# Performance work log

Measured on AMD Instinct MI355X. Metric: run time of the kernel, lower is better.

The kernel has to match this reference:

```python
import jax, jax.numpy as jnp
import numpy as np

N, E = 20000, 320000
IN_CH, HID, NPRED = 64, 512, 12
NUM_GCN = 3   # num_gcn_layers=4 -> 1 + (4-2) layers
NUM_RNN = 2
BN_EPS = 1e-5


def setup_inputs() -> dict:
    key = jax.random.key(0)
    ks = jax.random.split(key, 16)
    s = 0.05  # init scale to keep activations sane
    return {
        "x": jax.random.normal(ks[0], (N, IN_CH), jnp.float32),
        "edge_index": jax.random.randint(ks[1], (2, E), 0, N, jnp.int32),
        "edge_weight": jax.random.uniform(ks[2], (E,), jnp.float32),
        "gcn0_W": jax.random.normal(ks[3], (IN_CH, HID), jnp.float32) * s,
        "gcn0_b": jnp.zeros((HID,), jnp.float32),
        "gcn_W": jax.random.normal(ks[4], (NUM_GCN - 1, HID, HID), jnp.float32) * s,
        "gcn_b": jnp.zeros((NUM_GCN - 1, HID), jnp.float32),
        "bn_gamma": jnp.ones((NUM_GCN, HID), jnp.float32),
        "bn_beta": jnp.zeros((NUM_GCN, HID), jnp.float32),
        "w_ih": jax.random.normal(ks[5], (NUM_RNN, HID, 4 * HID), jnp.float32) * s,
        "w_hh": jax.random.normal(ks[6], (NUM_RNN, HID, 4 * HID), jnp.float32) * s,
        "w_ch": jax.random.normal(ks[7], (NUM_RNN, HID, 3 * HID), jnp.float32) * s,
        "lstm_b": jnp.zeros((NUM_RNN, 4 * HID), jnp.float32),
        "out_W": jax.random.normal(ks[8], (HID, NPRED), jnp.float32) * s,
        "out_b": jnp.zeros((NPRED,), jnp.float32),
    }


def _gcn(x, W, b, src, dst, ew, n):
    h = x @ W                                   # [N, out]
    msg = ew[:, None] * h[src]                  # [E, out]
    return jax.ops.segment_sum(msg, dst, num_segments=n) + b


def _bn_relu(x, gamma, beta):
    mu = jnp.mean(x, axis=0)
    var = jnp.var(x, axis=0)
    return jax.nn.relu((x - mu) * jax.lax.rsqrt(var + BN_EPS) * gamma + beta)


def _peephole_cell(inp, h, c, Wih, Whh, Wch, b):
    H = h.shape[1]
    gates = inp @ Wih + h @ Whh + b             # [N, 4H]
    i_g, f_g, g_g, o_g = jnp.split(gates, 4, axis=1)
    g_g = g_g + c @ Wch[:, :H]
    i_g = jax.nn.sigmoid(i_g)
    f_g = jax.nn.sigmoid(f_g + c @ Wch[:, H:2 * H])
    g_g = jnp.tanh(g_g)
    cy = f_g * c + i_g * g_g
    o_g = o_g + cy @ Wch[:, 2 * H:]
    hy = jax.nn.sigmoid(o_g) * jnp.tanh(cy)
    return hy, cy


def reference(x, edge_index, edge_weight, gcn0_W, gcn0_b, gcn_W, gcn_b,
              bn_gamma, bn_beta, w_ih, w_hh, w_ch, lstm_b, out_W, out_b):
    src, dst = edge_index[0], edge_index[1]
    n = x.shape[0]
    # GCN stack: conv -> batchnorm (train-mode stats) -> relu (dropout=0)
    h = _gcn(x, gcn0_W, gcn0_b, src, dst, edge_weight, n)
    h = _bn_relu(h, bn_gamma[0], bn_beta[0])
    for i in range(NUM_GCN - 1):
        h = _gcn(h, gcn_W[i], gcn_b[i], src, dst, edge_weight, n)
        h = _bn_relu(h, bn_gamma[i + 1], bn_beta[i + 1])
    # seq_len == 1 after unsqueeze; cells chained sharing (h_t, c_t)
    h_t = jnp.zeros((n, HID), h.dtype)
    c_t = jnp.zeros((n, HID), h.dtype)
    for l in range(NUM_RNN):
        h_t, c_t = _peephole_cell(h, h_t, c_t, w_ih[l], w_hh[l], w_ch[l], lstm_b[l])
    out = h_t @ out_W + out_b                   # [N, num_predictions]
    return jnp.squeeze(out)
```

## Files before the change

kernel.cpp:

```cpp
#include <hip/hip_runtime.h>
#include <cstddef>

#define N_NODES 20000
#define N_EDGES 320000
#define IN_CH   64
#define HID     512
#define G4      2048
#define BN_EPS  1e-5f
#define F_OFF   0
#define G_OFF   512
#define I_OFF   1024
#define O_OFF   1536

typedef __attribute__((ext_vector_type(8))) __bf16 bf16x8;
typedef __attribute__((ext_vector_type(4))) float f32x4;

__device__ __forceinline__ float sigmoidf_(float x) {
  return 1.0f / (1.0f + expf(-x));
}

__device__ __forceinline__ unsigned short f2b(float f) {
  unsigned int u = __float_as_uint(f);
  u += 0x7FFFu + ((u >> 16) & 1u);
  return (unsigned short)(u >> 16);
}
__device__ __forceinline__ float b2f(unsigned short u) {
  return __uint_as_float(((unsigned int)u) << 16);
}

__device__ __forceinline__ void gld_lds16(const unsigned short* g, unsigned short* l) {
  __builtin_amdgcn_global_load_lds(
      (const __attribute__((address_space(1))) unsigned int*)(const void*)g,
      (__attribute__((address_space(3))) unsigned int*)(void*)l, 16, 0, 0);
}

__global__ __launch_bounds__(256) void zero_k(float* __restrict__ p, size_t n) {
  size_t i = ((size_t)blockIdx.x * 256 + threadIdx.x) * 4;
  if (i + 3 < n) {
    *(float4*)&p[i] = make_float4(0.f, 0.f, 0.f, 0.f);
  } else {
    for (; i < n; i++) p[i] = 0.f;
  }
}

struct TcvtDesc { const float* W; unsigned short* Wt; int K, NC, ldw, ldo; };
struct TcvtBatch { TcvtDesc d[18]; };

__global__ void tcvtb_k(TcvtBatch batch) {
  const TcvtDesc dd = batch.d[blockIdx.z];
  __shared__ float tile[32][33];
  const int n0 = blockIdx.x * 32, k0 = blockIdx.y * 32;
  if (n0 >= dd.NC || k0 >= dd.K) return;
  const int tx = threadIdx.x, ty = threadIdx.y;
  #pragma unroll
  for (int i = 0; i < 32; i += 8) {
    int k = k0 + ty + i, n = n0 + tx;
    tile[ty + i][tx] = (k < dd.K && n < dd.NC) ? dd.W[(size_t)k * dd.ldw + n] : 0.f;
  }
  __syncthreads();
  #pragma unroll
  for (int i = 0; i < 32; i += 8) {
    int n = n0 + ty + i, k = k0 + tx;
    if (n < dd.NC && k < dd.K) dd.Wt[(size_t)n * dd.ldo + k] = f2b(tile[tx][ty + i]);
  }
}

__global__ __launch_bounds__(256) void hist_k(const int* __restrict__ dst,
                                              int* __restrict__ counts) {
  int e = blockIdx.x * 256 + threadIdx.x;
  if (e < N_EDGES) atomicAdd(&counts[dst[e]], 1);
}

__global__ __launch_bounds__(128) void scan1_k(const int* __restrict__ counts,
                                               int* __restrict__ offsets,
                                               int* __restrict__ bsum, int n) {
  __shared__ int sh[128];
  const int b = blockIdx.x, t = threadIdx.x;
  const int i = b * 128 + t;
  const int v = (i < n) ? counts[i] : 0;
  sh[t] = v;
  __syncthreads();
  #pragma unroll
  for (int off = 1; off < 128; off <<= 1) {
    int u = (t >= off) ? sh[t - off] : 0;
    __syncthreads();
    sh[t] += u;
    __syncthreads();
  }
  if (i < n) offsets[i] = sh[t] - v;
  if (t == 127) bsum[b] = sh[127];
}

__global__ __launch_bounds__(128) void scan2_k(const int* __restrict__ bsum,
                                               int* __restrict__ offsets,
                                               int* __restrict__ pos,
                                               int n, int nb) {
  __shared__ int red[128];
  __shared__ int base_s;
  const int b = blockIdx.x, t = threadIdx.x;
  int part = 0;
  if (t < b) part += bsum[t];
  if (t + 128 < b) part += bsum[t + 128];
  red[t] = part;
  __syncthreads();
  if (t < 64) {
    int v = red[t] + red[t + 64];
    #pragma unroll
    for (int off = 32; off > 0; off >>= 1) v += __shfl_down(v, off);
    if (t == 0) base_s = v;
  }
  __syncthreads();
  const int i = b * 128 + t;
  if (i < n) {
    int off = base_s + offsets[i];
    offsets[i] = off;
    pos[i] = off;
  }
  if (b == nb - 1 && t == 0) offsets[n] = base_s + bsum[b];
}

__global__ __launch_bounds__(256) void fill_k(
    const int* __restrict__ src, const int* __restrict__ dst,
    const float* __restrict__ ew, int* __restrict__ pos,
    int* __restrict__ s_s, float* __restrict__ w_s) {
  int e = blockIdx.x * 256 + threadIdx.x;
  if (e >= N_EDGES) return;
  int p = atomicAdd(&pos[dst[e]], 1);
  s_s[p] = src[e];
  w_s[p] = ew[e];
}

__global__ __launch_bounds__(64) void gather64_k(
    const float* __restrict__ x, const int* __restrict__ offsets,
    const int* __restrict__ s_s, const float* __restrict__ w_s,
    unsigned short* __restrict__ xg) {
  const int sub = threadIdx.x >> 4;
  const int cg  = threadIdx.x & 15;
  const int n   = blockIdx.x * 4 + sub;
  const int beg = offsets[n], end = offsets[n + 1];
  float4 acc = make_float4(0.f, 0.f, 0.f, 0.f);
  int i = beg;
  for (; i + 3 < end; i += 4) {
    const int   s0 = s_s[i],     s1 = s_s[i + 1];
    const int   s2 = s_s[i + 2], s3 = s_s[i + 3];
    const float w0 = w_s[i],     w1 = w_s[i + 1];
    const float w2 = w_s[i + 2], w3 = w_s[i + 3];
    const float4 v0 = *(const float4*)&x[(size_t)s0 * IN_CH + cg * 4];
    const float4 v1 = *(const float4*)&x[(size_t)s1 * IN_CH + cg * 4];
    const float4 v2 = *(const float4*)&x[(size_t)s2 * IN_CH + cg * 4];
    const float4 v3 = *(const float4*)&x[(size_t)s3 * IN_CH + cg * 4];
    acc.x = fmaf(w0, v0.x, acc.x); acc.y = fmaf(w0, v0.y, acc.y);
    acc.z = fmaf(w0, v0.z, acc.z); acc.w = fmaf(w0, v0.w, acc.w);
    acc.x = fmaf(w1, v1.x, acc.x); acc.y = fmaf(w1, v1.y, acc.y);
    acc.z = fmaf(w1, v1.z, acc.z); acc.w = fmaf(w1, v1.w, acc.w);
    acc.x = fmaf(w2, v2.x, acc.x); acc.y = fmaf(w2, v2.y, acc.y);
    acc.z = fmaf(w2, v2.z, acc.z); acc.w = fmaf(w2, v2.w, acc.w);
    acc.x = fmaf(w3, v3.x, acc.x); acc.y = fmaf(w3, v3.y, acc.y);
    acc.z = fmaf(w3, v3.z, acc.z); acc.w = fmaf(w3, v3.w, acc.w);
  }
  for (; i < end; i++) {
    const int   s = s_s[i];
    const float w = w_s[i];
    const float4 v = *(const float4*)&x[(size_t)s * IN_CH + cg * 4];
    acc.x = fmaf(w, v.x, acc.x);
    acc.y = fmaf(w, v.y, acc.y);
    acc.z = fmaf(w, v.z, acc.z);
    acc.w = fmaf(w, v.w, acc.w);
  }
  ushort4 o; o.x = f2b(acc.x); o.y = f2b(acc.y); o.z = f2b(acc.z); o.w = f2b(acc.w);
  *(ushort4*)&xg[(size_t)n * IN_CH + cg * 4] = o;
}

__global__ __launch_bounds__(128) void gather_k(
    const unsigned short* __restrict__ XW, const int* __restrict__ offsets,
    const int* __restrict__ s_s, const float* __restrict__ w_s,
    unsigned short* __restrict__ H) {
  const int n = blockIdx.x;
  const int t = threadIdx.x;
  const int beg = offsets[n], end = offsets[n + 1];
  float4 acc = make_float4(0.f, 0.f, 0.f, 0.f);
  int i = beg;
  for (; i + 3 < end; i += 4) {
    const int   s0 = s_s[i],     s1 = s_s[i + 1];
    const int   s2 = s_s[i + 2], s3 = s_s[i + 3];
    const float w0 = w_s[i],     w1 = w_s[i + 1];
    const float w2 = w_s[i + 2], w3 = w_s[i + 3];
    const ushort4 v0 = *(const ushort4*)&XW[(size_t)s0 * HID + t * 4];
    const ushort4 v1 = *(const ushort4*)&XW[(size_t)s1 * HID + t * 4];
    const ushort4 v2 = *(const ushort4*)&XW[(size_t)s2 * HID + t * 4];
    const ushort4 v3 = *(const ushort4*)&XW[(size_t)s3 * HID + t * 4];
    acc.x = fmaf(w0, b2f(v0.x), acc.x); acc.y = fmaf(w0, b2f(v0.y), acc.y);
    acc.z = fmaf(w0, b2f(v0.z), acc.z); acc.w = fmaf(w0, b2f(v0.w), acc.w);
    acc.x = fmaf(w1, b2f(v1.x), acc.x); acc.y = fmaf(w1, b2f(v1.y), acc.y);
    acc.z = fmaf(w1, b2f(v1.z), acc.z); acc.w = fmaf(w1, b2f(v1.w), acc.w);
    acc.x = fmaf(w2, b2f(v2.x), acc.x); acc.y = fmaf(w2, b2f(v2.y), acc.y);
    acc.z = fmaf(w2, b2f(v2.z), acc.z); acc.w = fmaf(w2, b2f(v2.w), acc.w);
    acc.x = fmaf(w3, b2f(v3.x), acc.x); acc.y = fmaf(w3, b2f(v3.y), acc.y);
    acc.z = fmaf(w3, b2f(v3.z), acc.z); acc.w = fmaf(w3, b2f(v3.w), acc.w);
  }
  for (; i < end; i++) {
    const int   s = s_s[i];
    const float w = w_s[i];
    const ushort4 v = *(const ushort4*)&XW[(size_t)s * HID + t * 4];
    acc.x = fmaf(w, b2f(v.x), acc.x);
    acc.y = fmaf(w, b2f(v.y), acc.y);
    acc.z = fmaf(w, b2f(v.z), acc.z);
    acc.w = fmaf(w, b2f(v.w), acc.w);
  }
  ushort4 o; o.x = f2b(acc.x); o.y = f2b(acc.y); o.z = f2b(acc.z); o.w = f2b(acc.w);
  *(ushort4*)&H[(size_t)n * HID + t * 4] = o;
}

__global__ __launch_bounds__(256) void bn_stats_k(
    const unsigned short* __restrict__ H, float* __restrict__ stats, int N)
{
  const int tx = threadIdx.x & 63;
  const int ty = threadIdx.x >> 6;
  const int col = blockIdx.x * 64 + tx;
  float s1 = 0.f, s2 = 0.f;
  for (int r = blockIdx.y * 4 + ty; r < N; r += gridDim.y * 4) {
    float v = b2f(H[(size_t)r * HID + col]);
    s1 += v; s2 += v * v;
  }
  __shared__ float red[2][4][64];
  red[0][ty][tx] = s1;
  red[1][ty][tx] = s2;
  __syncthreads();
  if (ty == 0) {
    s1 = red[0][0][tx] + red[0][1][tx] + red[0][2][tx] + red[0][3][tx];
    s2 = red[1][0][tx] + red[1][1][tx] + red[1][2][tx] + red[1][3][tx];
    atomicAdd(&stats[col], s1);
    atomicAdd(&stats[HID + col], s2);
  }
}

__global__ __launch_bounds__(256) void bn_apply_k(
    const unsigned short* __restrict__ H, const float* __restrict__ stats,
    const float* __restrict__ gamma, const float* __restrict__ beta,
    unsigned short* __restrict__ out, int N)
{
  size_t gid = (size_t)blockIdx.x * 256 + threadIdx.x;
  size_t idx = gid * 4;
  if (idx >= (size_t)N * HID) return;
  int col = (int)(idx & (HID - 1));
  const ushort4 v = *(const ushort4*)&H[idx];
  float r[4] = {b2f(v.x), b2f(v.y), b2f(v.z), b2f(v.w)};
  ushort4 o;
  unsigned short* op = &o.x;
  #pragma unroll
  for (int i = 0; i < 4; i++) {
    int c = col + i;
    float mean = stats[c] * (1.0f / N);
    float var  = stats[HID + c] * (1.0f / N) - mean * mean;
    float scale = gamma[c] / sqrtf(var + BN_EPS);
    float shift = beta[c] - mean * scale;
    op[i] = f2b(fmaxf(fmaf(r[i], scale, shift), 0.0f));
  }
  *(ushort4*)&out[idx] = o;
}

template<int BM, int BN>
__global__ __launch_bounds__(256) void gemm_bf16_k(
    const unsigned short* __restrict__ A, int lda,
    const unsigned short* __restrict__ A2, int lda2, int ksplit,
    const unsigned short* __restrict__ Bt,
    float* __restrict__ C, unsigned short* __restrict__ C16,
    const float* __restrict__ bias,
    int M, int K, int Ksmall, int NC, int ldc, int acc, int ntc,
    int nrowb, int ncolb)
{
  const int b   = blockIdx.x;
  const int xcd = b & 7;
  const int j   = b >> 3;
  const int col_b = j % ncolb;
  const int row_b = (j / ncolb) * 8 + xcd;
  if (row_b >= nrowb) return;

  constexpr int MI  = 2;
  constexpr int ASZ = BM * 64;
  constexpr int BSZ = BN * 64;
  __shared__ unsigned short As[2 * ASZ];
  __shared__ unsigned short Bs[2 * BSZ];
  const int row0 = row_b * BM;
  const int col0 = col_b * BN;
  const int Kthis = (col0 < 1024) ? K : Ksmall;
  const int t    = threadIdx.x;
  const int lane = t & 63;
  const int w    = t >> 6;
  const int wro  = (BN == 128) ? (w >> 1) * 32 : w * 32;
  const int wco  = (BN == 128) ? (w & 1) * 64 : 0;
  const int q    = lane >> 4;
  const int l16  = lane & 15;

  f32x4 accr[MI][4] = {};

  auto stage = [&](int buf, int k0) {
    unsigned short* Ad = As + buf * ASZ;
    unsigned short* Bd = Bs + buf * BSZ;
    #pragma unroll
    for (int i = 0; i < BM / 32; i++) {
      int s  = t + i * 256;
      int r  = s >> 3, cq = s & 7;
      int kq = (cq - r) & 7;
      int gr = row0 + r; if (gr > M - 1) gr = M - 1;
      int kk = k0 + kq * 8;
      const unsigned short* bp = (kk < ksplit) ? A : A2;
      size_t off = (kk < ksplit) ? ((size_t)gr * lda + kk)
                                 : ((size_t)gr * lda2 + (kk - ksplit));
      gld_lds16(bp + off, Ad + (size_t)s * 8);
    }
    #pragma unroll
    for (int i = 0; i < BN / 32; i++) {
      int s  = t + i * 256;
      int r  = s >> 3, cq = s & 7;
      int kq = (cq - r) & 7;
      gld_lds16(Bt + (size_t)(col0 + r) * K + k0 + kq * 8, Bd + (size_t)s * 8);
    }
  };

  stage(0, 0);
  int cur = 0;
  for (int k0 = 0; k0 < Kthis; k0 += 64) {
    __syncthreads();
    if (k0 + 64 < Kthis) stage(cur ^ 1, k0 + 64);

    const unsigned short* Ac = As + cur * ASZ;
    const unsigned short* Bc = Bs + cur * BSZ;
    #pragma unroll
    for (int ks = 0; ks < 2; ks++) {
      bf16x8 af[MI], bfr[4];
      #pragma unroll
      for (int mi = 0; mi < MI; mi++) {
        int r = wro + mi * 16 + l16;
        int slot = (ks * 4 + q + r) & 7;
        af[mi] = *(const bf16x8*)&Ac[r * 64 + slot * 8];
      }
      #pragma unroll
      for (int ni = 0; ni < 4; ni++) {
        int r = wco + ni * 16 + l16;
        int slot = (ks * 4 + q + r) & 7;
        bfr[ni] = *(const bf16x8*)&Bc[r * 64 + slot * 8];
      }
      #pragma unroll
      for (int mi = 0; mi < MI; mi++)
        #pragma unroll
        for (int ni = 0; ni < 4; ni++)
          accr[mi][ni] = __builtin_amdgcn_mfma_f32_16x16x32_bf16(
              af[mi], bfr[ni], accr[mi][ni], 0, 0, 0);
    }
    cur ^= 1;
  }

  #pragma unroll
  for (int mi = 0; mi < MI; mi++) {
    #pragma unroll
    for (int ni = 0; ni < 4; ni++) {
      int col = col0 + wco + ni * 16 + l16;
      #pragma unroll
      for (int r = 0; r < 4; r++) {
        int row = row0 + wro + mi * 16 + q * 4 + r;
        if (row < M) {
          float v = accr[mi][ni][r];
          if (C16) {
            unsigned short hv = f2b(v);
            unsigned short* hp = &C16[(size_t)row * ldc + col];
            if (ntc) __builtin_nontemporal_store(hv, hp);
            else     *hp = hv;
          } else {
            float* cp = &C[(size_t)row * ldc + col];
            if (acc)       *cp += v;
            else if (bias) *cp  = v + bias[col];
            else if (ntc)  __builtin_nontemporal_store(v, cp);
            else           *cp  = v;
          }
        }
      }
    }
  }
}

__global__ __launch_bounds__(256) void cell1_k(
    const unsigned short* __restrict__ gates, const float* __restrict__ lb,
    const float* __restrict__ cin,
    float* __restrict__ cout, unsigned short* __restrict__ cout16, int ld16,
    int rows, int hasC)
{
  size_t gid = (size_t)blockIdx.x * 256 + threadIdx.x;
  if (gid >= (size_t)rows * HID) return;
  size_t row = gid >> 9;
  int    col = (int)(gid & (HID - 1));
  const unsigned short* g = &gates[row * G4];
  float ig = sigmoidf_(b2f(__builtin_nontemporal_load(&g[I_OFF + col])) + lb[col]);
  float gg = tanhf(b2f(__builtin_nontemporal_load(&g[G_OFF + col])) + lb[2 * HID + col]);
  float c;
  if (hasC) {
    float fg = sigmoidf_(b2f(__builtin_nontemporal_load(&g[F_OFF + col])) + lb[HID + col]);
    c = fg * cin[gid] + ig * gg;
  } else {
    c = ig * gg;
  }
  cout[gid] = c;
  cout16[row * ld16 + col] = f2b(c);
}

__global__ __launch_bounds__(256) void cell2_k(
    const unsigned short* __restrict__ gates, const float* __restrict__ obuf,
    const float* __restrict__ lb, const float* __restrict__ cy,
    unsigned short* __restrict__ hy16, int ld16, int rows)
{
  size_t gid = (size_t)blockIdx.x * 256 + threadIdx.x;
  if (gid >= (size_t)rows * HID) return;
  size_t row = gid >> 9;
  int    col = (int)(gid & (HID - 1));
  float ov = b2f(__builtin_nontemporal_load(&gates[row * G4 + O_OFF + col]));
  float og = sigmoidf_(ov + obuf[gid] + lb[3 * HID + col]);
  float h = og * tanhf(cy[gid]);
  hy16[row * ld16 + col] = f2b(h);
}

__global__ __launch_bounds__(256) void cellout_k(
    const unsigned short* __restrict__ gates, const float* __restrict__ obuf,
    const float* __restrict__ lb, const float* __restrict__ cy,
    const float* __restrict__ W, const float* __restrict__ b,
    float* __restrict__ out, int rows)
{
  int wave = (int)(((size_t)blockIdx.x * 256 + threadIdx.x) >> 6);
  int lane = threadIdx.x & 63;
  if (wave >= rows) return;
  const unsigned short* g = &gates[(size_t)wave * G4 + O_OFF];
  const float* ob = &obuf[(size_t)wave * HID];
  const float* cr = &cy[(size_t)wave * HID];
  float hy[8];
  #pragma unroll
  for (int j = 0; j < 8; j++) {
    int k = lane + j * 64;
    float og = sigmoidf_(b2f(__builtin_nontemporal_load(&g[k])) + ob[k] + lb[3 * HID + k]);
    hy[j] = og * tanhf(cr[k]);
  }
  float acc[12] = {};
  #pragma unroll
  for (int j = 0; j < 8; j++) {
    int k = lane + j * 64;
    const float* wr = &W[k * 12];
    #pragma unroll
    for (int p = 0; p < 12; p++) acc[p] = fmaf(hy[j], wr[p], acc[p]);
  }
  #pragma unroll
  for (int p = 0; p < 12; p++) {
    float v = acc[p];
    #pragma unroll
    for (int off = 32; off > 0; off >>= 1) v += __shfl_down(v, off);
    if (lane == 0) out[(size_t)wave * 12 + p] = v + b[p];
  }
}

extern "C" void kernel_launch(void* const* d_in, const int* in_sizes, int n_in,
                              void* d_out, int out_size, void* d_ws, size_t ws_size,
                              hipStream_t stream) {
  const float* x     = (const float*)d_in[0];
  const int*   ei    = (const int*)d_in[1];
  const float* ew    = (const float*)d_in[2];
  const float* gcn0W = (const float*)d_in[3];
  const float* gcnW  = (const float*)d_in[5];
  const float* gamma = (const float*)d_in[7];
  const float* beta  = (const float*)d_in[8];
  const float* wih   = (const float*)d_in[9];
  const float* whh   = (const float*)d_in[10];
  const float* wch   = (const float*)d_in[11];
  const float* lstmb = (const float*)d_in[12];
  const float* outW  = (const float*)d_in[13];
  const float* outb  = (const float*)d_in[14];
  float* out = (float*)d_out;

  const int* src = ei;
  const int* dst = ei + N_EDGES;

  const int CH = (ws_size >= (size_t)215000000) ? 10000 : 5000;
  const int NCHUNK = N_NODES / CH;

  const size_t NH = (size_t)N_NODES * HID;
  float* ws = (float*)d_ws;
  float* gates = ws;
  float* bufH  = gates + (size_t)CH * G4;
  unsigned short* hbA16 = (unsigned short*)(bufH + NH);
  unsigned short* hbB16 = hbA16 + NH;
  unsigned short* x16   = hbB16 + NH;
  unsigned short* g0t   = x16 + (size_t)N_NODES * IN_CH;
  unsigned short* g1t   = g0t   + 512 * 64;
  unsigned short* g2t   = g1t   + 512 * 512;
  unsigned short* wih0t = g2t   + 512 * 512;
  unsigned short* wcat3 = wih0t + (size_t)1536 * 512;
  unsigned short* wch0ot= wcat3 + (size_t)2048 * 1536;
  unsigned short* wch1ot= wch0ot + 512 * 512;
  unsigned short* wend  = wch1ot + 512 * 512;
  unsigned short *a16, *tail16;
  if (CH == 5000) {
    a16  = hbB16;
    tail16 = wend;
  } else {
    a16  = wend;
    tail16 = a16 + (size_t)CH * 1024;
  }
  float* stats = (float*)tail16;
  int*   csr   = (int*)(stats + 3072);
  int*   counts  = csr;
  int*   offsets = csr + 20032;
  int*   cpos    = csr + 40064;
  int*   s_s     = csr + 60096;
  float* w_s     = (float*)(csr + 380096);
  int*   bsum    = (int*)x16;

  unsigned short* bufH16 = (unsigned short*)bufH;
  float* cbuf = bufH;
  float* obuf = bufH + (size_t)CH * HID;
  unsigned short* gates16 = (unsigned short*)gates;

  const dim3 blk(256);
  auto gemm128 = [&](const unsigned short* A, int lda,
                     const unsigned short* A2, int lda2, int ksplit,
                     const unsigned short* Bt, unsigned short* C16,
                     int M, int K, int Ksmall, int NC, int ldc) {
    int nrowb = (M + 63) / 64;
    int ncolb = NC / 128;
    int nblocks = 8 * ((nrowb + 7) / 8) * ncolb;
    hipLaunchKernelGGL((gemm_bf16_k<64, 128>), dim3(nblocks), blk, 0, stream,
                       A, lda, A2, lda2, ksplit, Bt, (float*)nullptr, C16,
                       (const float*)nullptr,
                       M, K, Ksmall, NC, ldc, 0, 1, nrowb, ncolb);
  };
  auto gemm64 = [&](const unsigned short* A, int lda,
                    const unsigned short* Bt, float* C, unsigned short* C16,
                    const float* bias, int M, int K, int NC, int ldc, int acc) {
    int nrowb = (M + 127) / 128;
    int ncolb = NC / 64;
    int nblocks = 8 * ((nrowb + 7) / 8) * ncolb;
    hipLaunchKernelGGL((gemm_bf16_k<128, 64>), dim3(nblocks), blk, 0, stream,
                       A, lda, A, lda, K, Bt, C, C16, bias,
                       M, K, K, NC, ldc, acc, 0, nrowb, ncolb);
  };
  auto zero = [&](float* p, size_t n) {
    hipLaunchKernelGGL(zero_k, dim3((unsigned)((n / 4 + 255) / 256)), blk, 0, stream, p, n);
  };

  const float* wih1 = wih + (size_t)HID * G4;
  const float* whh1 = whh + (size_t)HID * G4;
  const float* wch1 = wch + (size_t)HID * 3 * HID;
  {
    TcvtBatch tb;
    int n = 0;
    auto add = [&](const float* W, unsigned short* Wt, int K, int NC, int ldw, int ldo) {
      tb.d[n++] = TcvtDesc{W, Wt, K, NC, ldw, ldo};
    };
    add(gcn0W, g0t, IN_CH, HID, HID, IN_CH);
    add(gcnW,                     g1t, HID, HID, HID, HID);
    add(gcnW + (size_t)HID * HID, g2t, HID, HID, HID, HID);
    add(wih + 2 * HID, wih0t,                      HID, HID, G4, HID);
    add(wih,           wih0t + (size_t)512 * 512,  HID, HID, G4, HID);
    add(wih + 3 * HID, wih0t + (size_t)1024 * 512, HID, HID, G4, HID);
    add(wih1 + HID,     wcat3 + (size_t)F_OFF * 1536,        HID, HID, G4, 1536);
    add(whh1 + HID,     wcat3 + (size_t)F_OFF * 1536 + 512,  HID, HID, G4, 1536);
    add(wch1 + HID,     wcat3 + (size_t)F_OFF * 1536 + 1024, HID, HID, 3 * HID, 1536);
    add(wih1 + 2 * HID, wcat3 + (size_t)G_OFF * 1536,        HID, HID, G4, 1536);
    add(whh1 + 2 * HID, wcat3 + (size_t)G_OFF * 1536 + 512,  HID, HID, G4, 1536);
    add(wch1,           wcat3 + (size_t)G_OFF * 1536 + 1024, HID, HID, 3 * HID, 1536);
    add(wih1,           wcat3 + (size_t)I_OFF * 1536,        HID, HID, G4, 1536);
    add(whh1,           wcat3 + (size_t)I_OFF * 1536 + 512,  HID, HID, G4, 1536);
    add(wih1 + 3 * HID, wcat3 + (size_t)O_OFF * 1536,        HID, HID, G4, 1536);
    add(whh1 + 3 * HID, wcat3 + (size_t)O_OFF * 1536 + 512,  HID, HID, G4, 1536);
    add(wch + 2 * HID,  wch0ot, HID, HID, 3 * HID, HID);
    add(wch1 + 2 * HID, wch1ot, HID, HID, 3 * HID, HID);
    hipLaunchKernelGGL(tcvtb_k, dim3(16, 16, 18), dim3(32, 8), 0, stream, tb);
  }

  const int e_blocks = (N_EDGES + 255) / 256;
  const int nscanb = (N_NODES + 127) / 128;
  zero(stats, 3 * 1024 + N_NODES);
  hipLaunchKernelGGL(hist_k, dim3(e_blocks), blk, 0, stream, dst, counts);
  hipLaunchKernelGGL(scan1_k, dim3(nscanb), dim3(128), 0, stream,
                     counts, offsets, bsum, N_NODES);
  hipLaunchKernelGGL(scan2_k, dim3(nscanb), dim3(128), 0, stream,
                     bsum, offsets, cpos, N_NODES, nscanb);
  hipLaunchKernelGGL(fill_k, dim3(e_blocks), blk, 0, stream, src, dst, ew, cpos, s_s, w_s);

  hipLaunchKernelGGL(gather64_k, dim3(N_NODES / 4), dim3(64), 0, stream,
                     x, offsets, s_s, w_s, hbB16);
  gemm64(hbB16, IN_CH, g0t, nullptr, bufH16, nullptr, N_NODES, IN_CH, HID, HID, 0);
  hipLaunchKernelGGL(bn_stats_k, dim3(8, 64), blk, 0, stream, bufH16, stats, N_NODES);
  hipLaunchKernelGGL(bn_apply_k, dim3((unsigned)(NH / 4 / 256)), blk, 0, stream,
                     bufH16, stats, gamma, beta, hbA16, N_NODES);

  const unsigned short* gWt2[2] = {g1t, g2t};
  const unsigned short* gA2[2]  = {hbA16, hbB16};
  unsigned short*       gXW2[2] = {hbB16, hbA16};
  unsigned short*       gO2[2]  = {hbB16, hbA16};
  for (int l = 0; l < 2; l++) {
    gemm64(gA2[l], HID, gWt2[l], nullptr, gXW2[l], nullptr, N_NODES, HID, HID, HID, 0);
    hipLaunchKernelGGL(gather_k, dim3(N_NODES), dim3(128), 0, stream,
                       gXW2[l], offsets, s_s, w_s, bufH16);
    hipLaunchKernelGGL(bn_stats_k, dim3(8, 64), blk, 0, stream, bufH16,
                       stats + (l + 1) * 1024, N_NODES);
    hipLaunchKernelGGL(bn_apply_k, dim3((unsigned)(NH / 4 / 256)), blk, 0, stream,
                       bufH16, stats + (l + 1) * 1024, gamma + (l + 1) * HID,
                       beta + (l + 1) * HID, gO2[l], N_NODES);
  }
  unsigned short* hfin16 = hbA16;

  for (int ci = 0; ci < NCHUNK; ci++) {
    const int r0 = ci * CH;
    const unsigned short* h_c = hfin16 + (size_t)r0 * HID;
    const int cell_blocks = (int)(((size_t)CH * HID + 255) / 256);

    gemm128(h_c, HID, h_c, HID, HID, wih0t, gates16 + G_OFF,
            CH, HID, HID, 1536, G4);
    hipLaunchKernelGGL(cell1_k, dim3(cell_blocks), blk, 0, stream,
                       gates16, lstmb, (const float*)nullptr, cbuf, a16 + 512, 1024, CH, 0);
    gemm64(a16 + 512, 1024, wch0ot, obuf, nullptr, nullptr, CH, HID, HID, HID, 0);
    hipLaunchKernelGGL(cell2_k, dim3(cell_blocks), blk, 0, stream,
                       gates16, obuf, lstmb, cbuf, a16, 1024, CH);

    gemm128(h_c, HID, a16, 1024, HID, wcat3, gates16,
            CH, 1536, 1024, G4, G4);
    hipLaunchKernelGGL(cell1_k, dim3(cell_blocks), blk, 0, stream,
                       gates16, lstmb + G4, cbuf, cbuf, a16 + 512, 1024, CH, 1);
    gemm64(a16 + 512, 1024, wch1ot, obuf, nullptr, nullptr, CH, HID, HID, HID, 0);
    hipLaunchKernelGGL(cellout_k, dim3((CH * 64 + 255) / 256), blk, 0, stream,
                       gates16, obuf, lstmb + G4, cbuf, outW, outb,
                       out + (size_t)r0 * 12, CH);
  }
}
```

Measured before the change: 829.2 us.

## Store LSTM cell state and peephole output in bf16 and double chunk size

```diff
diff --git a/kernel.cpp b/kernel.cpp
--- a/kernel.cpp
+++ b/kernel.cpp
@@ -381,8 +381,8 @@
 
 __global__ __launch_bounds__(256) void cell1_k(
     const unsigned short* __restrict__ gates, const float* __restrict__ lb,
-    const float* __restrict__ cin,
-    float* __restrict__ cout, unsigned short* __restrict__ cout16, int ld16,
+    const unsigned short* __restrict__ cin16, int ldc16,
+    unsigned short* __restrict__ cout16, int ld16,
     int rows, int hasC)
 {
   size_t gid = (size_t)blockIdx.x * 256 + threadIdx.x;
@@ -395,17 +395,16 @@
   float c;
   if (hasC) {
     float fg = sigmoidf_(b2f(__builtin_nontemporal_load(&g[F_OFF + col])) + lb[HID + col]);
-    c = fg * cin[gid] + ig * gg;
+    c = fg * b2f(cin16[row * ldc16 + col]) + ig * gg;
   } else {
     c = ig * gg;
   }
-  cout[gid] = c;
   cout16[row * ld16 + col] = f2b(c);
 }
 
 __global__ __launch_bounds__(256) void cell2_k(
-    const unsigned short* __restrict__ gates, const float* __restrict__ obuf,
-    const float* __restrict__ lb, const float* __restrict__ cy,
+    const unsigned short* __restrict__ gates, const unsigned short* __restrict__ obuf16,
+    const float* __restrict__ lb, const unsigned short* __restrict__ cy16, int ldcy,
     unsigned short* __restrict__ hy16, int ld16, int rows)
 {
   size_t gid = (size_t)blockIdx.x * 256 + threadIdx.x;
@@ -413,29 +412,29 @@
   size_t row = gid >> 9;
   int    col = (int)(gid & (HID - 1));
   float ov = b2f(__builtin_nontemporal_load(&gates[row * G4 + O_OFF + col]));
-  float og = sigmoidf_(ov + obuf[gid] + lb[3 * HID + col]);
-  float h = og * tanhf(cy[gid]);
+  float og = sigmoidf_(ov + b2f(obuf16[row * HID + col]) + lb[3 * HID + col]);
+  float h = og * tanhf(b2f(cy16[row * ldcy + col]));
   hy16[row * ld16 + col] = f2b(h);
 }
 
 __global__ __launch_bounds__(256) void cellout_k(
-    const unsigned short* __restrict__ gates, const float* __restrict__ obuf,
-    const float* __restrict__ lb, const float* __restrict__ cy,
+    const unsigned short* __restrict__ gates, const unsigned short* __restrict__ obuf16,
+    const float* __restrict__ lb, const unsigned short* __restrict__ cy16, int ldcy,
     const float* __restrict__ W, const float* __restrict__ b,
     float* __restrict__ out, int rows)
 {
   int wave = (int)(((size_t)blockIdx.x * 256 + threadIdx.x) >> 6);
   int lane = threadIdx.x & 63;
   if (wave >= rows) return;
-  const unsigned short* g = &gates[(size_t)wave * G4 + O_OFF];
-  const float* ob = &obuf[(size_t)wave * HID];
-  const float* cr = &cy[(size_t)wave * HID];
+  const unsigned short* g  = &gates[(size_t)wave * G4 + O_OFF];
+  const unsigned short* ob = &obuf16[(size_t)wave * HID];
+  const unsigned short* cr = &cy16[(size_t)wave * ldcy];
   float hy[8];
   #pragma unroll
   for (int j = 0; j < 8; j++) {
     int k = lane + j * 64;
-    float og = sigmoidf_(b2f(__builtin_nontemporal_load(&g[k])) + ob[k] + lb[3 * HID + k]);
-    hy[j] = og * tanhf(cr[k]);
+    float og = sigmoidf_(b2f(__builtin_nontemporal_load(&g[k])) + b2f(ob[k]) + lb[3 * HID + k]);
+    hy[j] = og * tanhf(b2f(cr[k]));
   }
   float acc[12] = {};
   #pragma unroll
@@ -475,13 +474,14 @@
   const int* src = ei;
   const int* dst = ei + N_EDGES;
 
-  const int CH = (ws_size >= (size_t)215000000) ? 10000 : 5000;
+  const int CHL = (ws_size >= (size_t)215000000) ? 10000 : 5000;
+  const int CH  = 2 * CHL;
   const int NCHUNK = N_NODES / CH;
 
   const size_t NH = (size_t)N_NODES * HID;
   float* ws = (float*)d_ws;
   float* gates = ws;
-  float* bufH  = gates + (size_t)CH * G4;
+  float* bufH  = gates + (size_t)CHL * G4;
   unsigned short* hbA16 = (unsigned short*)(bufH + NH);
   unsigned short* hbB16 = hbA16 + NH;
   unsigned short* x16   = hbB16 + NH;
@@ -493,15 +493,7 @@
   unsigned short* wch0ot= wcat3 + (size_t)2048 * 1536;
   unsigned short* wch1ot= wch0ot + 512 * 512;
   unsigned short* wend  = wch1ot + 512 * 512;
-  unsigned short *a16, *tail16;
-  if (CH == 5000) {
-    a16  = hbB16;
-    tail16 = wend;
-  } else {
-    a16  = wend;
-    tail16 = a16 + (size_t)CH * 1024;
-  }
-  float* stats = (float*)tail16;
+  float* stats = (float*)wend;
   int*   csr   = (int*)(stats + 3072);
   int*   counts  = csr;
   int*   offsets = csr + 20032;
@@ -511,9 +503,9 @@
   int*   bsum    = (int*)x16;
 
   unsigned short* bufH16 = (unsigned short*)bufH;
-  float* cbuf = bufH;
-  float* obuf = bufH + (size_t)CH * HID;
   unsigned short* gates16 = (unsigned short*)gates;
+  unsigned short* a16     = (unsigned short*)bufH;
+  unsigned short* obuf16  = hbB16;
 
   const dim3 blk(256);
   auto gemm128 = [&](const unsigned short* A, int lda,
@@ -613,18 +605,20 @@
     gemm128(h_c, HID, h_c, HID, HID, wih0t, gates16 + G_OFF,
             CH, HID, HID, 1536, G4);
     hipLaunchKernelGGL(cell1_k, dim3(cell_blocks), blk, 0, stream,
-                       gates16, lstmb, (const float*)nullptr, cbuf, a16 + 512, 1024, CH, 0);
-    gemm64(a16 + 512, 1024, wch0ot, obuf, nullptr, nullptr, CH, HID, HID, HID, 0);
+                       gates16, lstmb, (const unsigned short*)nullptr, 0,
+                       a16 + 512, 1024, CH, 0);
+    gemm64(a16 + 512, 1024, wch0ot, nullptr, obuf16, nullptr, CH, HID, HID, HID, 0);
     hipLaunchKernelGGL(cell2_k, dim3(cell_blocks), blk, 0, stream,
-                       gates16, obuf, lstmb, cbuf, a16, 1024, CH);
+                       gates16, obuf16, lstmb, a16 + 512, 1024, a16, 1024, CH);
 
     gemm128(h_c, HID, a16, 1024, HID, wcat3, gates16,
             CH, 1536, 1024, G4, G4);
     hipLaunchKernelGGL(cell1_k, dim3(cell_blocks), blk, 0, stream,
-                       gates16, lstmb + G4, cbuf, cbuf, a16 + 512, 1024, CH, 1);
-    gemm64(a16 + 512, 1024, wch1ot, obuf, nullptr, nullptr, CH, HID, HID, HID, 0);
+                       gates16, lstmb + G4, a16 + 512, 1024,
+                       a16 + 512, 1024, CH, 1);
+    gemm64(a16 + 512, 1024, wch1ot, nullptr, obuf16, nullptr, CH, HID, HID, HID, 0);
     hipLaunchKernelGGL(cellout_k, dim3((CH * 64 + 255) / 256), blk, 0, stream,
-                       gates16, obuf, lstmb + G4, cbuf, outW, outb,
+                       gates16, obuf16, lstmb + G4, a16 + 512, 1024, outW, outb,
                        out + (size_t)r0 * 12, CH);
   }
 }
```

New measurement: 761.4 us. -8.2%, faster.
